# Performance work log

Measured on AMD Instinct MI355X. Metric: run time of the kernel, lower is better.

The kernel has to match this reference:

```python
import jax, jax.numpy as jnp
import numpy as np

NETS = 32
NODES = [256, 512, 512, 128]
BATCH = 4096


def setup_inputs() -> dict:
    key = jax.random.key(0)
    ks = jax.random.split(key, 7)
    def lin_init(k, n_out, n_in):
        # mimic nn.Linear default init scale
        bound = 1.0 / np.sqrt(n_in)
        kw, kb = jax.random.split(k)
        W = jax.random.uniform(kw, (NETS, n_out, n_in), jnp.float32, -bound, bound)
        b = jax.random.uniform(kb, (NETS, n_out), jnp.float32, -bound, bound)
        return W, b
    x = jax.random.normal(ks[0], (BATCH, NODES[0]), jnp.float32)
    W1, b1 = lin_init(ks[1], NODES[1], NODES[0])
    W2, b2 = lin_init(ks[2], NODES[2], NODES[1])
    W3, b3 = lin_init(ks[3], NODES[3], NODES[2])
    return {"x": x, "W1": W1, "b1": b1, "W2": W2, "b2": b2, "W3": W3, "b3": b3}


def reference(x, W1, b1, W2, b2, W3, b3):
    # Ensemble of independent MLPs expressed as batched GEMMs over the `nets` axis.
    # x: [B, in]; Wl: [N, out_l, in_l]; bl: [N, out_l]
    h = jax.nn.relu(jnp.einsum('bi,noi->bno', x, W1) + b1)        # [B, N, 512]
    h = jax.nn.relu(jnp.einsum('bni,noi->bno', h, W2) + b2)       # [B, N, 512]
    out = jnp.einsum('bni,noi->bno', h, W3) + b3                  # [B, N, 128] (identity act)
    B = x.shape[0]
    # Concatenate per-net outputs along feature dim: y[:, n*out_len:(n+1)*out_len]
    return out.reshape(B, -1)
```

## Files before the change

kernel.cpp:

```cpp
#include <hip/hip_runtime.h>

#define NETS 32
#define BATCH 4096
#define D0 256
#define D1 512
#define D2 512
#define D3 128
#define MT 64
#define LDA (D0 + 8)
#define LDH (D1 + 8)

using half8  = __attribute__((ext_vector_type(8))) _Float16;
using f32x16 = __attribute__((ext_vector_type(16))) float;

#define W1_N (NETS * D1 * D0)
#define W2_N (NETS * D2 * D1)
#define W3_N (NETS * D3 * D2)
#define X_N  (BATCH * D0)

template<int N, int K, int NI, int WSH>
__device__ __forceinline__ void cvt_w(const float* __restrict__ W, _Float16* __restrict__ Wh, int u) {
    constexpr int NKK = K / 16;
    const int t  = u % NKK;
    const int rg = u / NKK;
    const int n   = rg % N;
    const int net = rg / N;
    const int w  = n >> WSH;
    const int ni = (n >> 5) & (NI - 1);
    const int m  = n & 31;
    const float* src = W + (size_t)net * N * K + (size_t)n * K + t * 16;
    float4 v0 = *reinterpret_cast<const float4*>(src);
    float4 v1 = *reinterpret_cast<const float4*>(src + 4);
    float4 v2 = *reinterpret_cast<const float4*>(src + 8);
    float4 v3 = *reinterpret_cast<const float4*>(src + 12);
    half8 o0, o1;
    o0[0] = (_Float16)v0.x; o0[1] = (_Float16)v0.y; o0[2] = (_Float16)v0.z; o0[3] = (_Float16)v0.w;
    o0[4] = (_Float16)v1.x; o0[5] = (_Float16)v1.y; o0[6] = (_Float16)v1.z; o0[7] = (_Float16)v1.w;
    o1[0] = (_Float16)v2.x; o1[1] = (_Float16)v2.y; o1[2] = (_Float16)v2.z; o1[3] = (_Float16)v2.w;
    o1[4] = (_Float16)v3.x; o1[5] = (_Float16)v3.y; o1[6] = (_Float16)v3.z; o1[7] = (_Float16)v3.w;
    const int f = ((net * 4 + w) * NKK + t) * NI + ni;
    _Float16* dst = Wh + (size_t)f * 512 + m * 8;
    *reinterpret_cast<half8*>(dst)       = o0;
    *reinterpret_cast<half8*>(dst + 256) = o1;
}

__global__ void cvt_all(const float* __restrict__ x,
                        const float* __restrict__ W1, const float* __restrict__ W2,
                        const float* __restrict__ W3,
                        _Float16* __restrict__ Xh,
                        _Float16* __restrict__ W1h, _Float16* __restrict__ W2h,
                        _Float16* __restrict__ W3h) {
    const int i = blockIdx.x * blockDim.x + threadIdx.x;
    constexpr int TX = X_N / 16, T1 = W1_N / 16, T2 = W2_N / 16;
    if (i < TX) {
        const float* src = x + (size_t)i * 16;
        float4 v0 = *reinterpret_cast<const float4*>(src);
        float4 v1 = *reinterpret_cast<const float4*>(src + 4);
        float4 v2 = *reinterpret_cast<const float4*>(src + 8);
        float4 v3 = *reinterpret_cast<const float4*>(src + 12);
        half8 o0, o1;
        o0[0] = (_Float16)v0.x; o0[1] = (_Float16)v0.y; o0[2] = (_Float16)v0.z; o0[3] = (_Float16)v0.w;
        o0[4] = (_Float16)v1.x; o0[5] = (_Float16)v1.y; o0[6] = (_Float16)v1.z; o0[7] = (_Float16)v1.w;
        o1[0] = (_Float16)v2.x; o1[1] = (_Float16)v2.y; o1[2] = (_Float16)v2.z; o1[3] = (_Float16)v2.w;
        o1[4] = (_Float16)v3.x; o1[5] = (_Float16)v3.y; o1[6] = (_Float16)v3.z; o1[7] = (_Float16)v3.w;
        _Float16* dst = Xh + (size_t)i * 16;
        *reinterpret_cast<half8*>(dst)     = o0;
        *reinterpret_cast<half8*>(dst + 8) = o1;
    }
    else if (i < TX + T1)           cvt_w<D1, D0, 4, 7>(W1, W1h, i - TX);
    else if (i < TX + T1 + T2)      cvt_w<D2, D1, 4, 7>(W2, W2h, i - TX - T1);
    else                            cvt_w<D3, D2, 1, 5>(W3, W3h, i - TX - T1 - T2);
}

template<int K, int NI, int MI, int D>
__device__ __forceinline__ void layer32(const _Float16* As, int lda,
                                        const _Float16* __restrict__ wl,
                                        int lane_m, int oct,
                                        f32x16 (&acc)[MI][NI]) {
    constexpr int NKK = K / 16;
    half8 b[D + 1][NI];
#pragma unroll
    for (int d = 0; d < D; ++d)
#pragma unroll
        for (int ni = 0; ni < NI; ++ni)
            b[d][ni] = *reinterpret_cast<const half8*>(wl + (size_t)(d * NI + ni) * 512);
#pragma unroll
    for (int kk = 0; kk < NKK; ++kk) {
        if (kk + D < NKK) {
            const int slot = (kk + D) % (D + 1);
#pragma unroll
            for (int ni = 0; ni < NI; ++ni)
                b[slot][ni] = *reinterpret_cast<const half8*>(
                    wl + (size_t)((kk + D) * NI + ni) * 512);
        }
        half8 a[MI];
#pragma unroll
        for (int mi = 0; mi < MI; ++mi)
            a[mi] = *reinterpret_cast<const half8*>(
                As + (mi * 32 + lane_m) * lda + kk * 16 + oct * 8);
        const int cs = kk % (D + 1);
#pragma unroll
        for (int ni = 0; ni < NI; ++ni)
#pragma unroll
            for (int mi = 0; mi < MI; ++mi)
                acc[mi][ni] = __builtin_amdgcn_mfma_f32_32x32x16_f16(a[mi], b[cs][ni], acc[mi][ni], 0, 0, 0);
    }
}

template<int MI, int NI>
__device__ __forceinline__ void store_act32(f32x16 (&acc)[MI][NI], const float* __restrict__ bias,
                                            _Float16* dst, int ldd, int n_base,
                                            int lane_m, int oct) {
#pragma unroll
    for (int ni = 0; ni < NI; ++ni) {
        const int col = n_base + ni * 32 + lane_m;
        float bv = bias[col];
#pragma unroll
        for (int mi = 0; mi < MI; ++mi) {
#pragma unroll
            for (int r = 0; r < 16; ++r) {
                float v = acc[mi][ni][r] + bv;
                v = fmaxf(v, 0.0f);
                int row = mi * 32 + (r & 3) + 8 * (r >> 2) + 4 * oct;
                dst[row * ldd + col] = (_Float16)v;
            }
        }
    }
}

__global__ __launch_bounds__(256, 2) void mlp_fused(
    const _Float16* __restrict__ Xh,
    const _Float16* __restrict__ W1h, const float* __restrict__ b1,
    const _Float16* __restrict__ W2h, const float* __restrict__ b2,
    const _Float16* __restrict__ W3h, const float* __restrict__ b3,
    float* __restrict__ out) {
    __shared__ __align__(16) _Float16 buf[MT * LDH];

    const int tid = threadIdx.x;
    const int w = tid >> 6;
    const int l = tid & 63;
    const int lane_m = l & 31;
    const int oct = l >> 5;

    const int bb = blockIdx.x;
    const int xcd = bb & 7;
    const int s = bb >> 3;
    const int net = xcd * 4 + (s >> 6);
    const int mt = s & 63;
    const int m0 = mt * MT;

    {
        const _Float16* xsrc = Xh + (size_t)m0 * D0;
#pragma unroll
        for (int it = 0; it < 8; ++it) {
            int chunk = it * 256 + tid;
            int row = chunk >> 5;
            int c8 = chunk & 31;
            *reinterpret_cast<half8*>(&buf[row * LDA + c8 * 8]) =
                *reinterpret_cast<const half8*>(xsrc + row * D0 + c8 * 8);
        }
    }
    __syncthreads();

    {
        f32x16 acc[2][4] = {};
        const _Float16* wl = W1h + ((size_t)(net * 4 + w) * 64) * 512 + l * 8;
        layer32<D0, 4, 2, 2>(buf, LDA, wl, lane_m, oct, acc);
        __syncthreads();
        store_act32<2, 4>(acc, b1 + net * D1, buf, LDH, w * 128, lane_m, oct);
    }
    __syncthreads();

    {
        f32x16 acc[2][4] = {};
        const _Float16* wl = W2h + ((size_t)(net * 4 + w) * 128) * 512 + l * 8;
        layer32<D1, 4, 2, 2>(buf, LDH, wl, lane_m, oct, acc);
        __syncthreads();
        store_act32<2, 4>(acc, b2 + net * D2, buf, LDH, w * 128, lane_m, oct);
    }
    __syncthreads();

    {
        f32x16 acc[2][1] = {};
        const _Float16* wl = W3h + ((size_t)(net * 4 + w) * 32) * 512 + l * 8;
        layer32<D2, 1, 2, 8>(buf, LDH, wl, lane_m, oct, acc);
        const int col = net * D3 + w * 32 + lane_m;
        float bv = b3[net * D3 + w * 32 + lane_m];
#pragma unroll
        for (int mi = 0; mi < 2; ++mi) {
#pragma unroll
            for (int r = 0; r < 16; ++r) {
                int row = m0 + mi * 32 + (r & 3) + 8 * (r >> 2) + 4 * oct;
                out[(size_t)row * (NETS * D3) + col] = acc[mi][0][r] + bv;
            }
        }
    }
}

extern "C" void kernel_launch(void* const* d_in, const int* in_sizes, int n_in,
                              void* d_out, int out_size, void* d_ws, size_t ws_size,
                              hipStream_t stream) {
    const float* x  = (const float*)d_in[0];
    const float* W1 = (const float*)d_in[1];
    const float* b1 = (const float*)d_in[2];
    const float* W2 = (const float*)d_in[3];
    const float* b2 = (const float*)d_in[4];
    const float* W3 = (const float*)d_in[5];
    const float* b3 = (const float*)d_in[6];
    float* out = (float*)d_out;

    _Float16* Xh  = (_Float16*)d_ws;
    _Float16* W1h = Xh  + (size_t)X_N;
    _Float16* W2h = W1h + (size_t)W1_N;
    _Float16* W3h = W2h + (size_t)W2_N;

    const int totalT = (X_N + W1_N + W2_N + W3_N) / 16;
    cvt_all<<<totalT / 256, 256, 0, stream>>>(x, W1, W2, W3, Xh, W1h, W2h, W3h);

    mlp_fused<<<NETS * (BATCH / MT), 256, 0, stream>>>(Xh, W1h, b1, W2h, b2, W3h, b3, out);
}
```

Measured before the change: 244.7 us.

## Double the M tile to 128 rows with 8 waves sharing weight fragments

Doubles the batch tile per block to 128 rows and launches 512-thread blocks. Two groups of four waves each take one 64-row half and read the same weight fragments, which halves the block count and the total weight traffic pulled from L2 per batch row. The weight-conversion kernel also changes its thread-to-element mapping so that the fp16 stores are coalesced, at the price of strided fp32 reads. The larger LDS buffer (about 133KB) likely limits each CU to one resident block.

```diff
diff --git a/kernel.cpp b/kernel.cpp
--- a/kernel.cpp
+++ b/kernel.cpp
@@ -6,7 +6,7 @@
 #define D1 512
 #define D2 512
 #define D3 128
-#define MT 64
+#define MT 128
 #define LDA (D0 + 8)
 #define LDH (D1 + 8)
 
@@ -18,17 +18,19 @@
 #define W3_N (NETS * D3 * D2)
 #define X_N  (BATCH * D0)
 
-template<int N, int K, int NI, int WSH>
+template<int N, int K, int NI>
 __device__ __forceinline__ void cvt_w(const float* __restrict__ W, _Float16* __restrict__ Wh, int u) {
     constexpr int NKK = K / 16;
-    const int t  = u % NKK;
-    const int rg = u / NKK;
-    const int n   = rg % N;
-    const int net = rg / N;
-    const int w  = n >> WSH;
-    const int ni = (n >> 5) & (NI - 1);
-    const int m  = n & 31;
-    const float* src = W + (size_t)net * N * K + (size_t)n * K + t * 16;
+    const int m  = u & 31;
+    const int f  = u >> 5;
+    const int ni = f % NI;
+    const int rest = f / NI;
+    const int kk = rest % NKK;
+    const int g  = rest / NKK;
+    const int wn = g & 3;
+    const int net = g >> 2;
+    const int n = wn * (NI * 32) + ni * 32 + m;
+    const float* src = W + (size_t)net * N * K + (size_t)n * K + kk * 16;
     float4 v0 = *reinterpret_cast<const float4*>(src);
     float4 v1 = *reinterpret_cast<const float4*>(src + 4);
     float4 v2 = *reinterpret_cast<const float4*>(src + 8);
@@ -38,7 +40,6 @@
     o0[4] = (_Float16)v1.x; o0[5] = (_Float16)v1.y; o0[6] = (_Float16)v1.z; o0[7] = (_Float16)v1.w;
     o1[0] = (_Float16)v2.x; o1[1] = (_Float16)v2.y; o1[2] = (_Float16)v2.z; o1[3] = (_Float16)v2.w;
     o1[4] = (_Float16)v3.x; o1[5] = (_Float16)v3.y; o1[6] = (_Float16)v3.z; o1[7] = (_Float16)v3.w;
-    const int f = ((net * 4 + w) * NKK + t) * NI + ni;
     _Float16* dst = Wh + (size_t)f * 512 + m * 8;
     *reinterpret_cast<half8*>(dst)       = o0;
     *reinterpret_cast<half8*>(dst + 256) = o1;
@@ -67,9 +68,9 @@
         *reinterpret_cast<half8*>(dst)     = o0;
         *reinterpret_cast<half8*>(dst + 8) = o1;
     }
-    else if (i < TX + T1)           cvt_w<D1, D0, 4, 7>(W1, W1h, i - TX);
-    else if (i < TX + T1 + T2)      cvt_w<D2, D1, 4, 7>(W2, W2h, i - TX - T1);
-    else                            cvt_w<D3, D2, 1, 5>(W3, W3h, i - TX - T1 - T2);
+    else if (i < TX + T1)           cvt_w<D1, D0, 4>(W1, W1h, i - TX);
+    else if (i < TX + T1 + T2)      cvt_w<D2, D1, 4>(W2, W2h, i - TX - T1);
+    else                            cvt_w<D3, D2, 1>(W3, W3h, i - TX - T1 - T2);
 }
 
 template<int K, int NI, int MI, int D>
@@ -128,7 +129,7 @@
     }
 }
 
-__global__ __launch_bounds__(256, 2) void mlp_fused(
+__global__ __launch_bounds__(512, 2) void mlp_fused(
     const _Float16* __restrict__ Xh,
     const _Float16* __restrict__ W1h, const float* __restrict__ b1,
     const _Float16* __restrict__ W2h, const float* __restrict__ b2,
@@ -138,6 +139,8 @@
 
     const int tid = threadIdx.x;
     const int w = tid >> 6;
+    const int wn = w & 3;
+    const int wm = w >> 2;
     const int l = tid & 63;
     const int lane_m = l & 31;
     const int oct = l >> 5;
@@ -145,15 +148,15 @@
     const int bb = blockIdx.x;
     const int xcd = bb & 7;
     const int s = bb >> 3;
-    const int net = xcd * 4 + (s >> 6);
-    const int mt = s & 63;
+    const int net = xcd * 4 + (s >> 5);
+    const int mt = s & 31;
     const int m0 = mt * MT;
 
     {
         const _Float16* xsrc = Xh + (size_t)m0 * D0;
 #pragma unroll
         for (int it = 0; it < 8; ++it) {
-            int chunk = it * 256 + tid;
+            int chunk = it * 512 + tid;
             int row = chunk >> 5;
             int c8 = chunk & 31;
             *reinterpret_cast<half8*>(&buf[row * LDA + c8 * 8]) =
@@ -164,33 +167,33 @@
 
     {
         f32x16 acc[2][4] = {};
-        const _Float16* wl = W1h + ((size_t)(net * 4 + w) * 64) * 512 + l * 8;
-        layer32<D0, 4, 2, 2>(buf, LDA, wl, lane_m, oct, acc);
+        const _Float16* wl = W1h + ((size_t)(net * 4 + wn) * 64) * 512 + l * 8;
+        layer32<D0, 4, 2, 2>(buf + wm * 64 * LDA, LDA, wl, lane_m, oct, acc);
         __syncthreads();
-        store_act32<2, 4>(acc, b1 + net * D1, buf, LDH, w * 128, lane_m, oct);
+        store_act32<2, 4>(acc, b1 + net * D1, buf + wm * 64 * LDH, LDH, wn * 128, lane_m, oct);
     }
     __syncthreads();
 
     {
         f32x16 acc[2][4] = {};
-        const _Float16* wl = W2h + ((size_t)(net * 4 + w) * 128) * 512 + l * 8;
-        layer32<D1, 4, 2, 2>(buf, LDH, wl, lane_m, oct, acc);
+        const _Float16* wl = W2h + ((size_t)(net * 4 + wn) * 128) * 512 + l * 8;
+        layer32<D1, 4, 2, 2>(buf + wm * 64 * LDH, LDH, wl, lane_m, oct, acc);
         __syncthreads();
-        store_act32<2, 4>(acc, b2 + net * D2, buf, LDH, w * 128, lane_m, oct);
+        store_act32<2, 4>(acc, b2 + net * D2, buf + wm * 64 * LDH, LDH, wn * 128, lane_m, oct);
     }
     __syncthreads();
 
     {
         f32x16 acc[2][1] = {};
-        const _Float16* wl = W3h + ((size_t)(net * 4 + w) * 32) * 512 + l * 8;
-        layer32<D2, 1, 2, 8>(buf, LDH, wl, lane_m, oct, acc);
-        const int col = net * D3 + w * 32 + lane_m;
-        float bv = b3[net * D3 + w * 32 + lane_m];
+        const _Float16* wl = W3h + ((size_t)(net * 4 + wn) * 32) * 512 + l * 8;
+        layer32<D2, 1, 2, 8>(buf + wm * 64 * LDH, LDH, wl, lane_m, oct, acc);
+        const int col = net * D3 + wn * 32 + lane_m;
+        float bv = b3[net * D3 + wn * 32 + lane_m];
 #pragma unroll
         for (int mi = 0; mi < 2; ++mi) {
 #pragma unroll
             for (int r = 0; r < 16; ++r) {
-                int row = m0 + mi * 32 + (r & 3) + 8 * (r >> 2) + 4 * oct;
+                int row = m0 + wm * 64 + mi * 32 + (r & 3) + 8 * (r >> 2) + 4 * oct;
                 out[(size_t)row * (NETS * D3) + col] = acc[mi][0][r] + bv;
             }
         }
@@ -217,5 +220,5 @@
     const int totalT = (X_N + W1_N + W2_N + W3_N) / 16;
     cvt_all<<<totalT / 256, 256, 0, stream>>>(x, W1, W2, W3, Xh, W1h, W2h, W3h);
 
-    mlp_fused<<<NETS * (BATCH / MT), 256, 0, stream>>>(Xh, W1h, b1, W2h, b2, W3h, b3, out);
-}
+    mlp_fused<<<NETS * (BATCH / MT), 512, 0, stream>>>(Xh, W1h, b1, W2h, b2, W3h, b3, out);
+}
```

Result: slower. 252.6 us (+3.2%).
